# Performance work log

Hardware: AMD Instinct MI355X
Metric: run time of the kernel (lower is better)

## Reference

```python
import jax, jax.numpy as jnp
import numpy as np

N_NODES = 50000
N_EDGES = 800000
N_GRAPHS = 50
D_IN = 128
D_HID = 128
D_OUT = 10


def setup_inputs() -> dict:
    key = jax.random.key(0)
    ks = jax.random.split(key, 8)
    h = jax.random.normal(ks[0], (N_NODES, D_IN), dtype=jnp.float32)
    src = jax.random.randint(ks[1], (N_EDGES,), 0, N_NODES, dtype=jnp.int32)
    dst = jax.random.randint(ks[2], (N_EDGES,), 0, N_NODES, dtype=jnp.int32)
    graph_ids = jnp.sort(jax.random.randint(ks[3], (N_NODES,), 0, N_GRAPHS, dtype=jnp.int32))
    s = 1.0 / np.sqrt(D_HID)
    W1 = jax.random.normal(ks[4], (D_IN, D_HID), dtype=jnp.float32) * s
    W2 = jax.random.normal(ks[5], (D_HID, D_HID), dtype=jnp.float32) * s
    W3 = jax.random.normal(ks[6], (D_HID, D_HID), dtype=jnp.float32) * s
    Wm = jax.random.normal(ks[7], (D_HID, D_OUT), dtype=jnp.float32) * s
    return {
        "h": h, "src": src, "dst": dst, "graph_ids": graph_ids,
        "W1": W1, "b1": jnp.zeros((D_HID,), jnp.float32),
        "W2": W2, "b2": jnp.zeros((D_HID,), jnp.float32),
        "W3": W3, "b3": jnp.zeros((D_HID,), jnp.float32),
        "Wm": Wm, "bm": jnp.zeros((D_OUT,), jnp.float32),
    }


def _graph_conv(h, W, b, src, dst, norm_src, norm_dst):
    # DGL GraphConv, norm='both': out = D_dst^{-1/2} * A @ (D_src^{-1/2} * h) @ W + b
    m = (h * norm_src[:, None])[src]              # [E, d] gather (memory-bound)
    agg = jax.ops.segment_sum(m, dst, num_segments=N_NODES)  # [N, d] scatter-add
    return (agg * norm_dst[:, None]) @ W + b


def reference(h, src, dst, graph_ids, W1, b1, W2, b2, W3, b3, Wm, bm):
    ones_e = jnp.ones((N_EDGES,), jnp.float32)
    out_deg = jax.ops.segment_sum(ones_e, src, num_segments=N_NODES)
    in_deg = jax.ops.segment_sum(ones_e, dst, num_segments=N_NODES)
    norm_src = jnp.clip(out_deg, 1.0, None) ** -0.5
    norm_dst = jnp.clip(in_deg, 1.0, None) ** -0.5

    h = jax.nn.relu(_graph_conv(h, W1, b1, src, dst, norm_src, norm_dst))
    h = jax.nn.relu(_graph_conv(h, W2, b2, src, dst, norm_src, norm_dst))
    h = jax.nn.relu(_graph_conv(h, W3, b3, src, dst, norm_src, norm_dst))

    # mean-nodes readout per graph
    hg_sum = jax.ops.segment_sum(h, graph_ids, num_segments=N_GRAPHS)  # [G, d]
    cnt = jax.ops.segment_sum(jnp.ones((N_NODES,), jnp.float32), graph_ids, num_segments=N_GRAPHS)
    hg = hg_sum / jnp.clip(cnt, 1.0, None)[:, None]

    logits = hg @ Wm + bm                                 # [G, D_OUT]
    return jax.nn.log_softmax(logits, axis=0)             # faithful to dim=0 in source
```

## Files before the change

### kernel.cpp

```cpp
#include <hip/hip_runtime.h>

#define N_NODES 50000
#define N_EDGES 800000
#define N_GRAPHS 50
#define D 128
#define D_OUT 10
#define PLANE_F4 200000
#define NSH 8

__global__ __launch_bounds__(256) void hist8_k(const int* __restrict__ src,
                                               const int* __restrict__ dst,
                                               int* __restrict__ cnt8,
                                               int* __restrict__ cs8) {
    int i = blockIdx.x * 256 + threadIdx.x;
    int sh = (blockIdx.x & (NSH - 1)) * N_NODES;
    if (i < N_EDGES) {
        atomicAdd(&cnt8[sh + dst[i]], 1);
        atomicAdd(&cs8[sh + src[i]], 1);
    }
}

__global__ __launch_bounds__(256) void scanA_k(const int* __restrict__ cnt8,
                                               int* __restrict__ bs) {
    int b = blockIdx.x, t = threadIdx.x;
    int n = b * 196 + t;
    int v = 0;
    if (t < 196 && n < N_NODES) {
        #pragma unroll
        for (int x = 0; x < NSH; x++) v += cnt8[x * N_NODES + n];
    }
    __shared__ int wsum[4];
    int lane = t & 63, wid = t >> 6;
    #pragma unroll
    for (int d = 32; d; d >>= 1) v += __shfl_down(v, d, 64);
    if (lane == 0) wsum[wid] = v;
    __syncthreads();
    if (t == 0) bs[b] = wsum[0] + wsum[1] + wsum[2] + wsum[3];
}

__global__ __launch_bounds__(256) void scanB_k(int* __restrict__ bs) {
    int t = threadIdx.x;
    int v = bs[t];
    int lane = t & 63, wid = t >> 6;
    __shared__ int wsum[4];
    int x = v;
    #pragma unroll
    for (int d = 1; d < 64; d <<= 1) {
        int y = __shfl_up(x, d, 64);
        if (lane >= d) x += y;
    }
    if (lane == 63) wsum[wid] = x;
    __syncthreads();
    int add = 0;
    #pragma unroll
    for (int i = 0; i < 4; i++) if (i < wid) add += wsum[i];
    bs[t] = add + x - v;
}

__global__ __launch_bounds__(256) void scanC_k(int* __restrict__ cnt8,
                                               const int* __restrict__ cs8,
                                               const int* __restrict__ bs,
                                               int* __restrict__ row_ptr,
                                               float* __restrict__ ns,
                                               float* __restrict__ nd) {
    int b = blockIdx.x, t = threadIdx.x;
    int n = b * 196 + t;
    bool act = (t < 196) && (n < N_NODES);
    int c[NSH];
    int v = 0;
    if (act) {
        #pragma unroll
        for (int x = 0; x < NSH; x++) { c[x] = cnt8[x * N_NODES + n]; v += c[x]; }
    }
    int lane = t & 63, wid = t >> 6;
    __shared__ int wsum[4];
    int xv = v;
    #pragma unroll
    for (int d = 1; d < 64; d <<= 1) {
        int y = __shfl_up(xv, d, 64);
        if (lane >= d) xv += y;
    }
    if (lane == 63) wsum[wid] = xv;
    __syncthreads();
    int add = 0;
    #pragma unroll
    for (int i = 0; i < 4; i++) if (i < wid) add += wsum[i];
    int excl = bs[b] + add + xv - v;
    if (act) {
        row_ptr[n] = excl;
        int rb = excl;
        #pragma unroll
        for (int x = 0; x < NSH; x++) { cnt8[x * N_NODES + n] = rb; rb += c[x]; }
        int od = 0;
        #pragma unroll
        for (int x = 0; x < NSH; x++) od += cs8[x * N_NODES + n];
        ns[n] = 1.0f / sqrtf((float)(od > 1 ? od : 1));
        nd[n] = 1.0f / sqrtf((float)(v > 1 ? v : 1));
    }
    if (b == 255 && t == 0) row_ptr[N_NODES] = N_EDGES;
}

__global__ __launch_bounds__(256) void scatter8_k(const int* __restrict__ src,
                                                  const int* __restrict__ dst,
                                                  int* __restrict__ cursor8,
                                                  unsigned short* __restrict__ col) {
    int i = blockIdx.x * 256 + threadIdx.x;
    int sh = (blockIdx.x & (NSH - 1)) * N_NODES;
    if (i < N_EDGES) {
        int s = src[i];
        int d = dst[i];
        int p = atomicAdd(&cursor8[sh + d], 1);
        col[p] = (unsigned short)s;
    }
}

__global__ __launch_bounds__(256) void prescale_k(const float* __restrict__ h,
                                                  const float* __restrict__ ns,
                                                  float* __restrict__ out) {
    int i = blockIdx.x * 256 + threadIdx.x;
    if (i < N_NODES * 32) {
        int node = i >> 5;
        int kg = i & 31;
        float4 v = ((const float4*)h)[i];
        float s = ns[node];
        int p = kg >> 2, q = kg & 3;
        ((float4*)out)[p * PLANE_F4 + node * 4 + q] =
            make_float4(v.x * s, v.y * s, v.z * s, v.w * s);
    }
}

__global__ __launch_bounds__(256) void spmm_k(const float* __restrict__ x,
                                              const int* __restrict__ row_ptr,
                                              const unsigned short* __restrict__ col,
                                              const float* __restrict__ nd,
                                              float* __restrict__ out) {
    int b = blockIdx.x;
    int slice = b & 7;
    int node = (b >> 3) * 64 + (threadIdx.x >> 2);
    if (node >= N_NODES) return;
    int q = threadIdx.x & 3;
    int s = row_ptr[node];
    int e = row_ptr[node + 1];
    const float4* xp = (const float4*)x + slice * PLANE_F4;
    float4 a0 = make_float4(0.f, 0.f, 0.f, 0.f);
    float4 a1 = make_float4(0.f, 0.f, 0.f, 0.f);
    int i = s;
    for (; i + 4 <= e; i += 4) {
        int c0 = col[i], c1 = col[i + 1], c2 = col[i + 2], c3 = col[i + 3];
        float4 h0 = xp[c0 * 4 + q];
        float4 h1 = xp[c1 * 4 + q];
        float4 h2 = xp[c2 * 4 + q];
        float4 h3 = xp[c3 * 4 + q];
        a0.x += h0.x; a0.y += h0.y; a0.z += h0.z; a0.w += h0.w;
        a1.x += h1.x; a1.y += h1.y; a1.z += h1.z; a1.w += h1.w;
        a0.x += h2.x; a0.y += h2.y; a0.z += h2.z; a0.w += h2.w;
        a1.x += h3.x; a1.y += h3.y; a1.z += h3.z; a1.w += h3.w;
    }
    for (; i < e; i++) {
        float4 hv = xp[col[i] * 4 + q];
        a0.x += hv.x; a0.y += hv.y; a0.z += hv.z; a0.w += hv.w;
    }
    float ndv = nd[node];
    ((float4*)out)[slice * PLANE_F4 + node * 4 + q] =
        make_float4((a0.x + a1.x) * ndv, (a0.y + a1.y) * ndv,
                    (a0.z + a1.z) * ndv, (a0.w + a1.w) * ndv);
}

template <int MODE>
__global__ __launch_bounds__(512) void gemm_relu_k(const float* __restrict__ A,
                                                   const float* __restrict__ W,
                                                   const float* __restrict__ bias,
                                                   const float* __restrict__ ns,
                                                   float* __restrict__ out) {
    __shared__ float As_t[128 * 256];
    int tid = threadIdx.x;
    int row0 = blockIdx.x * 256;
    const float4* A4 = (const float4*)A;

    #pragma unroll
    for (int it = 0; it < 16; it++) {
        int linear = it * 512 + tid;
        int p = linear >> 10;
        int rem = linear & 1023;
        int r = rem >> 2;
        int q = rem & 3;
        int row = row0 + r;
        float4 a = (row < N_NODES) ? A4[p * PLANE_F4 + row * 4 + q]
                                   : make_float4(0.f, 0.f, 0.f, 0.f);
        int kb = p * 16 + q * 4;
        As_t[(kb + 0) * 256 + r] = a.x;
        As_t[(kb + 1) * 256 + r] = a.y;
        As_t[(kb + 2) * 256 + r] = a.z;
        As_t[(kb + 3) * 256 + r] = a.w;
    }
    __syncthreads();

    int tc = tid & 15;
    int tr = tid >> 4;
    float acc[8][8];
    #pragma unroll
    for (int r = 0; r < 8; r++)
        #pragma unroll
        for (int c = 0; c < 8; c++) acc[r][c] = 0.f;

    const float4* W4 = (const float4*)W;
    #pragma unroll 2
    for (int k = 0; k < 128; k++) {
        float4 w0 = W4[k * 32 + tc * 2];
        float4 w1 = W4[k * 32 + tc * 2 + 1];
        float4 a0 = *(const float4*)(As_t + k * 256 + tr * 8);
        float4 a1 = *(const float4*)(As_t + k * 256 + tr * 8 + 4);
        float av[8] = {a0.x, a0.y, a0.z, a0.w, a1.x, a1.y, a1.z, a1.w};
        float wv[8] = {w0.x, w0.y, w0.z, w0.w, w1.x, w1.y, w1.z, w1.w};
        #pragma unroll
        for (int rr = 0; rr < 8; rr++)
            #pragma unroll
            for (int cc = 0; cc < 8; cc++)
                acc[rr][cc] = fmaf(av[rr], wv[cc], acc[rr][cc]);
    }

    float4 bv0 = ((const float4*)bias)[tc * 2];
    float4 bv1 = ((const float4*)bias)[tc * 2 + 1];
    #pragma unroll
    for (int rr = 0; rr < 8; rr++) {
        int row = row0 + tr * 8 + rr;
        if (row < N_NODES) {
            float4 o0, o1;
            o0.x = fmaxf(acc[rr][0] + bv0.x, 0.f);
            o0.y = fmaxf(acc[rr][1] + bv0.y, 0.f);
            o0.z = fmaxf(acc[rr][2] + bv0.z, 0.f);
            o0.w = fmaxf(acc[rr][3] + bv0.w, 0.f);
            o1.x = fmaxf(acc[rr][4] + bv1.x, 0.f);
            o1.y = fmaxf(acc[rr][5] + bv1.y, 0.f);
            o1.z = fmaxf(acc[rr][6] + bv1.z, 0.f);
            o1.w = fmaxf(acc[rr][7] + bv1.w, 0.f);
            if (MODE == 0) {
                float s = ns[row];
                o0.x *= s; o0.y *= s; o0.z *= s; o0.w *= s;
                o1.x *= s; o1.y *= s; o1.z *= s; o1.w *= s;
                int p = tc >> 1;
                int q0 = (tc & 1) * 2;
                ((float4*)out)[p * PLANE_F4 + row * 4 + q0] = o0;
                ((float4*)out)[p * PLANE_F4 + row * 4 + q0 + 1] = o1;
            } else {
                ((float4*)out)[row * 32 + tc * 2] = o0;
                ((float4*)out)[row * 32 + tc * 2 + 1] = o1;
            }
        }
    }
}

__global__ __launch_bounds__(256) void proj_readout_k(const float* __restrict__ h,
                                                      const int* __restrict__ gid,
                                                      const float* __restrict__ Wm,
                                                      float* __restrict__ hgp,
                                                      int* __restrict__ gcnt) {
    __shared__ float Wmt[10 * 144];
    int tid = threadIdx.x;
    for (int i = tid; i < 1280; i += 256) {
        int k = i / 10, o = i % 10;
        Wmt[o * 144 + k + 4 * (k >> 5)] = Wm[i];
    }
    __syncthreads();

    int v = blockIdx.x * 64 + (tid >> 2);
    int quarter = tid & 3;
    int lane = tid & 63;

    float acc[D_OUT];
    #pragma unroll
    for (int o = 0; o < D_OUT; o++) acc[o] = 0.f;
    int g = -1;
    int cnt = 0;
    if (v < N_NODES) {
        g = gid[v];
        cnt = (quarter == 0) ? 1 : 0;
        const float4* h4 = (const float4*)h + v * 32 + quarter * 8;
        const float* wbase = Wmt + quarter * 36;
        #pragma unroll
        for (int kk = 0; kk < 8; kk++) {
            float4 hv = h4[kk];
            #pragma unroll
            for (int o = 0; o < D_OUT; o++) {
                float4 w = *(const float4*)(wbase + o * 144 + kk * 4);
                acc[o] += hv.x * w.x + hv.y * w.y + hv.z * w.z + hv.w * w.w;
            }
        }
    }

    #pragma unroll
    for (int d = 1; d < 64; d <<= 1) {
        int gp = __shfl_up(g, d, 64);
        int cp = __shfl_up(cnt, d, 64);
        bool take = (lane >= d) && (gp == g);
        #pragma unroll
        for (int o = 0; o < D_OUT; o++) {
            float ap = __shfl_up(acc[o], d, 64);
            if (take) acc[o] += ap;
        }
        if (take) cnt += cp;
    }
    int gn = __shfl_down(g, 1, 64);
    bool tail = (lane == 63) || (gn != g);
    if (tail && g >= 0) {
        #pragma unroll
        for (int o = 0; o < D_OUT; o++) atomicAdd(&hgp[g * D_OUT + o], acc[o]);
        if (cnt > 0) atomicAdd(&gcnt[g], cnt);
    }
}

__global__ __launch_bounds__(512) void final_k(const float* __restrict__ hgp,
                                               const int* __restrict__ gcnt,
                                               const float* __restrict__ bm,
                                               float* __restrict__ out) {
    __shared__ float lg[N_GRAPHS * D_OUT];
    __shared__ float colm[D_OUT], colls[D_OUT];
    int tid = threadIdx.x;
    if (tid < N_GRAPHS * D_OUT) {
        int g = tid / D_OUT, o = tid % D_OUT;
        float c = (float)gcnt[g];
        lg[tid] = hgp[tid] / (c > 1.f ? c : 1.f) + bm[o];
    }
    __syncthreads();
    if (tid < D_OUT) {
        float m = -1e30f;
        for (int g = 0; g < N_GRAPHS; g++) m = fmaxf(m, lg[g * D_OUT + tid]);
        float s = 0.f;
        for (int g = 0; g < N_GRAPHS; g++) s += expf(lg[g * D_OUT + tid] - m);
        colm[tid] = m; colls[tid] = logf(s);
    }
    __syncthreads();
    if (tid < N_GRAPHS * D_OUT) {
        int o = tid % D_OUT;
        out[tid] = lg[tid] - colm[o] - colls[o];
    }
}

extern "C" void kernel_launch(void* const* d_in, const int* in_sizes, int n_in,
                              void* d_out, int out_size, void* d_ws, size_t ws_size,
                              hipStream_t stream) {
    const float* h_in = (const float*)d_in[0];
    const int*   src  = (const int*)d_in[1];
    const int*   dst  = (const int*)d_in[2];
    const int*   gid  = (const int*)d_in[3];
    const float* W1 = (const float*)d_in[4];  const float* b1 = (const float*)d_in[5];
    const float* W2 = (const float*)d_in[6];  const float* b2 = (const float*)d_in[7];
    const float* W3 = (const float*)d_in[8];  const float* b3 = (const float*)d_in[9];
    const float* Wm = (const float*)d_in[10]; const float* bm = (const float*)d_in[11];

    char* ws = (char*)d_ws;
    int*            row_ptr = (int*)(ws + 0);
    unsigned short* col16   = (unsigned short*)(ws + 200032);
    float*          ns      = (float*)(ws + 1800032);
    float*          nd      = (float*)(ws + 2000032);
    int*            gcnt    = (int*)(ws + 2200032);
    float*          hgp     = (float*)(ws + 2200288);
    int*            bs      = (int*)(ws + 2202336);
    float*          bufA    = (float*)(ws + 2203360);
    float*          bufB    = (float*)(ws + 27803360);
    int*            cnt8    = (int*)bufA;
    int*            cs8     = (int*)bufB;

    hipMemsetAsync(ws + 2200032, 0, 2304, stream);
    hipMemsetAsync(cnt8, 0, 1600000, stream);
    hipMemsetAsync(cs8, 0, 1600000, stream);

    hist8_k<<<3125, 256, 0, stream>>>(src, dst, cnt8, cs8);
    scanA_k<<<256, 256, 0, stream>>>(cnt8, bs);
    scanB_k<<<1, 256, 0, stream>>>(bs);
    scanC_k<<<256, 256, 0, stream>>>(cnt8, cs8, bs, row_ptr, ns, nd);
    scatter8_k<<<3125, 256, 0, stream>>>(src, dst, cnt8, col16);
    prescale_k<<<6250, 256, 0, stream>>>(h_in, ns, bufA);

    spmm_k<<<6256, 256, 0, stream>>>(bufA, row_ptr, col16, nd, bufB);
    gemm_relu_k<0><<<196, 512, 0, stream>>>(bufB, W1, b1, ns, bufA);
    spmm_k<<<6256, 256, 0, stream>>>(bufA, row_ptr, col16, nd, bufB);
    gemm_relu_k<0><<<196, 512, 0, stream>>>(bufB, W2, b2, ns, bufA);
    spmm_k<<<6256, 256, 0, stream>>>(bufA, row_ptr, col16, nd, bufB);
    gemm_relu_k<1><<<196, 512, 0, stream>>>(bufB, W3, b3, ns, bufA);

    proj_readout_k<<<782, 256, 0, stream>>>(bufA, gid, Wm, hgp, gcnt);
    final_k<<<1, 512, 0, stream>>>(hgp, gcnt, bm, (float*)d_out);
}
```

Before: 523.2 us.

## Build CSR via two-level bucket partition with LDS-local counting sort

Replaces the sharded global-atomic histogram, three-kernel scan and atomic scatter with a bucketed counting sort. Edges are first partitioned into buckets of 256 destination nodes using per-block LDS histograms and a single scan. Each bucket is then sorted in LDS to produce row_ptr, col16 and the destination norms. The source normalization is recomputed from integer out-degrees wherever it is used instead of being stored as a separate array. The goal is to cut global atomic traffic and kernel launches; the cost is a hard cap of 8192 edges per bucket and only 196 blocks per partition kernel.

```diff
diff --git a/kernel.cpp b/kernel.cpp
--- a/kernel.cpp
+++ b/kernel.cpp
@@ -6,123 +6,159 @@
 #define D 128
 #define D_OUT 10
 #define PLANE_F4 200000
-#define NSH 8
-
-__global__ __launch_bounds__(256) void hist8_k(const int* __restrict__ src,
-                                               const int* __restrict__ dst,
-                                               int* __restrict__ cnt8,
-                                               int* __restrict__ cs8) {
-    int i = blockIdx.x * 256 + threadIdx.x;
-    int sh = (blockIdx.x & (NSH - 1)) * N_NODES;
-    if (i < N_EDGES) {
-        atomicAdd(&cnt8[sh + dst[i]], 1);
-        atomicAdd(&cs8[sh + src[i]], 1);
-    }
-}
-
-__global__ __launch_bounds__(256) void scanA_k(const int* __restrict__ cnt8,
-                                               int* __restrict__ bs) {
-    int b = blockIdx.x, t = threadIdx.x;
-    int n = b * 196 + t;
-    int v = 0;
-    if (t < 196 && n < N_NODES) {
-        #pragma unroll
-        for (int x = 0; x < NSH; x++) v += cnt8[x * N_NODES + n];
-    }
-    __shared__ int wsum[4];
-    int lane = t & 63, wid = t >> 6;
-    #pragma unroll
-    for (int d = 32; d; d >>= 1) v += __shfl_down(v, d, 64);
-    if (lane == 0) wsum[wid] = v;
-    __syncthreads();
-    if (t == 0) bs[b] = wsum[0] + wsum[1] + wsum[2] + wsum[3];
-}
-
-__global__ __launch_bounds__(256) void scanB_k(int* __restrict__ bs) {
-    int t = threadIdx.x;
-    int v = bs[t];
-    int lane = t & 63, wid = t >> 6;
-    __shared__ int wsum[4];
+#define NB 196
+#define NBLK 196
+
+__global__ __launch_bounds__(256) void part_hist_src(const int* __restrict__ src,
+                                                     const int* __restrict__ dst,
+                                                     int* __restrict__ gh,
+                                                     int* __restrict__ out_deg) {
+    __shared__ int lh[NB];
+    int tid = threadIdx.x, blk = blockIdx.x;
+    if (tid < NB) lh[tid] = 0;
+    __syncthreads();
+    int base = blk * 4096;
+    #pragma unroll
+    for (int j = 0; j < 16; j++) {
+        int i = base + j * 256 + tid;
+        if (i < N_EDGES) {
+            atomicAdd(&out_deg[src[i]], 1);
+            atomicAdd(&lh[dst[i] >> 8], 1);
+        }
+    }
+    __syncthreads();
+    if (tid < NB) gh[tid * NBLK + blk] = lh[tid];
+}
+
+__global__ __launch_bounds__(1024) void part_scan(int* __restrict__ gh) {
+    __shared__ int wsum[16];
+    __shared__ int carry_s;
+    const int N = NB * NBLK;
+    int tid = threadIdx.x;
+    int lane = tid & 63, wid = tid >> 6;
+    if (tid == 0) carry_s = 0;
+    __syncthreads();
+    for (int base = 0; base < N; base += 4096) {
+        int i0 = base + tid * 4;
+        int v0 = (i0 + 0 < N) ? gh[i0 + 0] : 0;
+        int v1 = (i0 + 1 < N) ? gh[i0 + 1] : 0;
+        int v2 = (i0 + 2 < N) ? gh[i0 + 2] : 0;
+        int v3 = (i0 + 3 < N) ? gh[i0 + 3] : 0;
+        int s = v0 + v1 + v2 + v3;
+        int x = s;
+        #pragma unroll
+        for (int d = 1; d < 64; d <<= 1) {
+            int y = __shfl_up(x, d, 64);
+            if (lane >= d) x += y;
+        }
+        if (lane == 63) wsum[wid] = x;
+        __syncthreads();
+        if (wid == 0) {
+            int t = (lane < 16) ? wsum[lane] : 0;
+            #pragma unroll
+            for (int d = 1; d < 16; d <<= 1) {
+                int y = __shfl_up(t, d, 64);
+                if (lane >= d) t += y;
+            }
+            if (lane < 16) wsum[lane] = t;
+        }
+        __syncthreads();
+        int woff = (wid == 0) ? 0 : wsum[wid - 1];
+        int run = carry_s + woff + (x - s);
+        if (i0 + 0 < N) gh[i0 + 0] = run; run += v0;
+        if (i0 + 1 < N) gh[i0 + 1] = run; run += v1;
+        if (i0 + 2 < N) gh[i0 + 2] = run; run += v2;
+        if (i0 + 3 < N) gh[i0 + 3] = run; run += v3;
+        __syncthreads();
+        if (tid == 0) carry_s += wsum[15];
+        __syncthreads();
+    }
+}
+
+__global__ __launch_bounds__(256) void part_scatter(const int* __restrict__ src,
+                                                    const int* __restrict__ dst,
+                                                    const int* __restrict__ gh,
+                                                    unsigned int* __restrict__ packed) {
+    __shared__ int lc[NB];
+    int tid = threadIdx.x, blk = blockIdx.x;
+    if (tid < NB) lc[tid] = gh[tid * NBLK + blk];
+    __syncthreads();
+    int base = blk * 4096;
+    #pragma unroll
+    for (int j = 0; j < 16; j++) {
+        int i = base + j * 256 + tid;
+        if (i < N_EDGES) {
+            int d = dst[i];
+            int s = src[i];
+            int p = atomicAdd(&lc[d >> 8], 1);
+            packed[p] = ((unsigned int)(d & 255) << 16) | (unsigned int)s;
+        }
+    }
+}
+
+__global__ __launch_bounds__(256) void bucket_csr(const unsigned int* __restrict__ packed,
+                                                  const int* __restrict__ gh,
+                                                  unsigned short* __restrict__ col16,
+                                                  int* __restrict__ row_ptr,
+                                                  float* __restrict__ nd) {
+    __shared__ unsigned int ep[8192];
+    __shared__ unsigned short lcol[8192];
+    __shared__ int hist[256], cur[256], wsum[4];
+    int t = threadIdx.x, b = blockIdx.x;
+    int nb = gh[b * NBLK];
+    int ne = (b < NB - 1) ? gh[(b + 1) * NBLK] : N_EDGES;
+    int cnt = ne - nb;
+    if (cnt > 8192) cnt = 8192;
+    hist[t] = 0;
+    __syncthreads();
+    for (int i = t; i < cnt; i += 256) {
+        unsigned int e = packed[nb + i];
+        ep[i] = e;
+        atomicAdd(&hist[e >> 16], 1);
+    }
+    __syncthreads();
+    int v = hist[t];
+    int lane = t & 63, w = t >> 6;
     int x = v;
     #pragma unroll
     for (int d = 1; d < 64; d <<= 1) {
         int y = __shfl_up(x, d, 64);
         if (lane >= d) x += y;
     }
-    if (lane == 63) wsum[wid] = x;
+    if (lane == 63) wsum[w] = x;
     __syncthreads();
     int add = 0;
     #pragma unroll
-    for (int i = 0; i < 4; i++) if (i < wid) add += wsum[i];
-    bs[t] = add + x - v;
-}
-
-__global__ __launch_bounds__(256) void scanC_k(int* __restrict__ cnt8,
-                                               const int* __restrict__ cs8,
-                                               const int* __restrict__ bs,
-                                               int* __restrict__ row_ptr,
-                                               float* __restrict__ ns,
-                                               float* __restrict__ nd) {
-    int b = blockIdx.x, t = threadIdx.x;
-    int n = b * 196 + t;
-    bool act = (t < 196) && (n < N_NODES);
-    int c[NSH];
-    int v = 0;
-    if (act) {
-        #pragma unroll
-        for (int x = 0; x < NSH; x++) { c[x] = cnt8[x * N_NODES + n]; v += c[x]; }
-    }
-    int lane = t & 63, wid = t >> 6;
-    __shared__ int wsum[4];
-    int xv = v;
-    #pragma unroll
-    for (int d = 1; d < 64; d <<= 1) {
-        int y = __shfl_up(xv, d, 64);
-        if (lane >= d) xv += y;
-    }
-    if (lane == 63) wsum[wid] = xv;
-    __syncthreads();
-    int add = 0;
-    #pragma unroll
-    for (int i = 0; i < 4; i++) if (i < wid) add += wsum[i];
-    int excl = bs[b] + add + xv - v;
-    if (act) {
-        row_ptr[n] = excl;
-        int rb = excl;
-        #pragma unroll
-        for (int x = 0; x < NSH; x++) { cnt8[x * N_NODES + n] = rb; rb += c[x]; }
-        int od = 0;
-        #pragma unroll
-        for (int x = 0; x < NSH; x++) od += cs8[x * N_NODES + n];
-        ns[n] = 1.0f / sqrtf((float)(od > 1 ? od : 1));
-        nd[n] = 1.0f / sqrtf((float)(v > 1 ? v : 1));
-    }
-    if (b == 255 && t == 0) row_ptr[N_NODES] = N_EDGES;
-}
-
-__global__ __launch_bounds__(256) void scatter8_k(const int* __restrict__ src,
-                                                  const int* __restrict__ dst,
-                                                  int* __restrict__ cursor8,
-                                                  unsigned short* __restrict__ col) {
-    int i = blockIdx.x * 256 + threadIdx.x;
-    int sh = (blockIdx.x & (NSH - 1)) * N_NODES;
-    if (i < N_EDGES) {
-        int s = src[i];
-        int d = dst[i];
-        int p = atomicAdd(&cursor8[sh + d], 1);
-        col[p] = (unsigned short)s;
-    }
+    for (int i = 0; i < 4; i++) if (i < w) add += wsum[i];
+    int excl = add + x - v;
+    cur[t] = excl;
+    int node = b * 256 + t;
+    if (node < N_NODES) {
+        row_ptr[node] = nb + excl;
+        int id = v > 1 ? v : 1;
+        nd[node] = 1.0f / sqrtf((float)id);
+    }
+    if (b == NB - 1 && t == 0) row_ptr[N_NODES] = N_EDGES;
+    __syncthreads();
+    for (int i = t; i < cnt; i += 256) {
+        unsigned int e = ep[i];
+        int p = atomicAdd(&cur[e >> 16], 1);
+        lcol[p] = (unsigned short)(e & 0xFFFF);
+    }
+    __syncthreads();
+    for (int i = t; i < cnt; i += 256) col16[nb + i] = lcol[i];
 }
 
 __global__ __launch_bounds__(256) void prescale_k(const float* __restrict__ h,
-                                                  const float* __restrict__ ns,
+                                                  const int* __restrict__ out_deg,
                                                   float* __restrict__ out) {
     int i = blockIdx.x * 256 + threadIdx.x;
     if (i < N_NODES * 32) {
         int node = i >> 5;
         int kg = i & 31;
         float4 v = ((const float4*)h)[i];
-        float s = ns[node];
+        int od = out_deg[node];
+        float s = 1.0f / sqrtf((float)(od > 1 ? od : 1));
         int p = kg >> 2, q = kg & 3;
         ((float4*)out)[p * PLANE_F4 + node * 4 + q] =
             make_float4(v.x * s, v.y * s, v.z * s, v.w * s);
@@ -170,7 +206,7 @@
 __global__ __launch_bounds__(512) void gemm_relu_k(const float* __restrict__ A,
                                                    const float* __restrict__ W,
                                                    const float* __restrict__ bias,
-                                                   const float* __restrict__ ns,
+                                                   const int* __restrict__ odeg,
                                                    float* __restrict__ out) {
     __shared__ float As_t[128 * 256];
     int tid = threadIdx.x;
@@ -235,7 +271,8 @@
             o1.z = fmaxf(acc[rr][6] + bv1.z, 0.f);
             o1.w = fmaxf(acc[rr][7] + bv1.w, 0.f);
             if (MODE == 0) {
-                float s = ns[row];
+                int od = odeg[row];
+                float s = 1.0f / sqrtf((float)(od > 1 ? od : 1));
                 o0.x *= s; o0.y *= s; o0.z *= s; o0.w *= s;
                 o1.x *= s; o1.y *= s; o1.z *= s; o1.w *= s;
                 int p = tc >> 1;
@@ -351,33 +388,30 @@
     char* ws = (char*)d_ws;
     int*            row_ptr = (int*)(ws + 0);
     unsigned short* col16   = (unsigned short*)(ws + 200032);
-    float*          ns      = (float*)(ws + 1800032);
+    int*            out_deg = (int*)(ws + 1800032);
     float*          nd      = (float*)(ws + 2000032);
     int*            gcnt    = (int*)(ws + 2200032);
     float*          hgp     = (float*)(ws + 2200288);
-    int*            bs      = (int*)(ws + 2202336);
-    float*          bufA    = (float*)(ws + 2203360);
-    float*          bufB    = (float*)(ws + 27803360);
-    int*            cnt8    = (int*)bufA;
-    int*            cs8     = (int*)bufB;
-
-    hipMemsetAsync(ws + 2200032, 0, 2304, stream);
-    hipMemsetAsync(cnt8, 0, 1600000, stream);
-    hipMemsetAsync(cs8, 0, 1600000, stream);
-
-    hist8_k<<<3125, 256, 0, stream>>>(src, dst, cnt8, cs8);
-    scanA_k<<<256, 256, 0, stream>>>(cnt8, bs);
-    scanB_k<<<1, 256, 0, stream>>>(bs);
-    scanC_k<<<256, 256, 0, stream>>>(cnt8, cs8, bs, row_ptr, ns, nd);
-    scatter8_k<<<3125, 256, 0, stream>>>(src, dst, cnt8, col16);
-    prescale_k<<<6250, 256, 0, stream>>>(h_in, ns, bufA);
+    int*            gh      = (int*)(ws + 2202336);
+    float*          bufA    = (float*)(ws + 2356000);
+    float*          bufB    = (float*)(ws + 27956000);
+    unsigned int*   packed  = (unsigned int*)bufB;
+
+    hipMemsetAsync(out_deg, 0, 200000, stream);
+    hipMemsetAsync(gcnt, 0, 2304, stream);
+
+    part_hist_src<<<NBLK, 256, 0, stream>>>(src, dst, gh, out_deg);
+    part_scan<<<1, 1024, 0, stream>>>(gh);
+    part_scatter<<<NBLK, 256, 0, stream>>>(src, dst, gh, packed);
+    bucket_csr<<<NB, 256, 0, stream>>>(packed, gh, col16, row_ptr, nd);
+    prescale_k<<<6250, 256, 0, stream>>>(h_in, out_deg, bufA);
 
     spmm_k<<<6256, 256, 0, stream>>>(bufA, row_ptr, col16, nd, bufB);
-    gemm_relu_k<0><<<196, 512, 0, stream>>>(bufB, W1, b1, ns, bufA);
+    gemm_relu_k<0><<<196, 512, 0, stream>>>(bufB, W1, b1, out_deg, bufA);
     spmm_k<<<6256, 256, 0, stream>>>(bufA, row_ptr, col16, nd, bufB);
-    gemm_relu_k<0><<<196, 512, 0, stream>>>(bufB, W2, b2, ns, bufA);
+    gemm_relu_k<0><<<196, 512, 0, stream>>>(bufB, W2, b2, out_deg, bufA);
     spmm_k<<<6256, 256, 0, stream>>>(bufA, row_ptr, col16, nd, bufB);
-    gemm_relu_k<1><<<196, 512, 0, stream>>>(bufB, W3, b3, ns, bufA);
+    gemm_relu_k<1><<<196, 512, 0, stream>>>(bufB, W3, b3, out_deg, bufA);
 
     proj_readout_k<<<782, 256, 0, stream>>>(bufA, gid, Wm, hgp, gcnt);
     final_k<<<1, 512, 0, stream>>>(hgp, gcnt, bm, (float*)d_out);
```

Result: faster. 474.4 us (-9.3%).
